# Kernel optimization log

Hardware: AMD Instinct MI355X
Metric: run time of the kernel (lower is better)

## Reference

```python
import jax, jax.numpy as jnp
import numpy as np

B, S, D, H = 4, 2048, 1024, 16
HS = D // H  # head_size = 64


def setup_inputs() -> dict:
    key = jax.random.key(0)
    ks = jax.random.split(key, 6)
    scale = 0.02
    return {
        "token_embeddings": jax.random.normal(ks[0], (B, S, D), dtype=jnp.float32),
        # per-head projection weights, stacked: [H, D, HS] (x @ W per head)
        "Wq": jax.random.normal(ks[1], (H, D, HS), dtype=jnp.float32) * scale,
        "Wk": jax.random.normal(ks[2], (H, D, HS), dtype=jnp.float32) * scale,
        "Wv": jax.random.normal(ks[3], (H, D, HS), dtype=jnp.float32) * scale,
        # output projection (Linear with bias): y = x @ Wo + bo
        "Wo": jax.random.normal(ks[4], (D, D), dtype=jnp.float32) * scale,
        "bo": jax.random.normal(ks[5], (D,), dtype=jnp.float32) * scale,
    }


def reference(token_embeddings, Wq, Wk, Wv, Wo, bo):
    # Per-head projections, batched over heads: [B,H,S,HS]
    q = jnp.einsum("bsd,hde->bhse", token_embeddings, Wq)
    k = jnp.einsum("bsd,hde->bhse", token_embeddings, Wk)
    v = jnp.einsum("bsd,hde->bhse", token_embeddings, Wv)
    scale = HS ** -0.5
    scores = jnp.einsum("bhqe,bhke->bhqk", q, k) * scale  # [B,H,S,S]
    causal = jnp.tril(jnp.ones((S, S), dtype=bool))
    scores = jnp.where(causal, scores, -jnp.inf)
    weights = jax.nn.softmax(scores, axis=-1)
    # dropout in eval mode -> identity
    out = jnp.einsum("bhqk,bhke->bhqe", weights, v)  # [B,H,S,HS]
    # concat heads -> [B,S,D] (head order matches torch.cat over heads)
    out = out.transpose(0, 2, 1, 3).reshape(B, S, D)
    return out @ Wo + bo
```

## Files before the change

kernel.cpp:

```cpp
#include <hip/hip_runtime.h>


typedef __bf16 bf16;
typedef bf16 bf16x8 __attribute__((ext_vector_type(8)));
typedef bf16 bf16x4 __attribute__((ext_vector_type(4)));
typedef float f32x4 __attribute__((ext_vector_type(4)));

__device__ __forceinline__ void gload16(const void* gsrc, void* ldst) {
  __builtin_amdgcn_global_load_lds(
      (const __attribute__((address_space(1))) unsigned int*)gsrc,
      (__attribute__((address_space(3))) unsigned int*)ldst, 16, 0, 0);
}

__device__ __forceinline__ f32x4 mfma16(bf16x8 a, bf16x8 b, f32x4 c) {
  return __builtin_amdgcn_mfma_f32_16x16x32_bf16(a, b, c, 0, 0, 0);
}

__global__ __launch_bounds__(256) void pack_x_kernel(const float* __restrict__ x,
                                                     bf16* __restrict__ xb) {
  int i = (blockIdx.x * 256 + threadIdx.x) * 4;
  float4 v = *(const float4*)(x + i);
  bf16x4 o;
  o[0] = (bf16)v.x; o[1] = (bf16)v.y; o[2] = (bf16)v.z; o[3] = (bf16)v.w;
  *(bf16x4*)(xb + i) = o;
}

__global__ __launch_bounds__(256) void pack_wqkv_kernel(const float* __restrict__ Wq,
                                                        const float* __restrict__ Wk,
                                                        const float* __restrict__ Wv,
                                                        bf16* __restrict__ WT) {
  int idx = blockIdx.x * 256 + threadIdx.x;
  int n = idx >> 10, k = idx & 1023;
  int sel = n >> 10, nn = n & 1023;
  const float* W = (sel == 0) ? Wq : (sel == 1 ? Wk : Wv);
  int h = nn >> 6, e = nn & 63;
  WT[(size_t)n * 1024 + k] = (bf16)W[h * 65536 + k * 64 + e];
}

__global__ __launch_bounds__(256) void pack_wo_kernel(const float* __restrict__ Wo,
                                                      bf16* __restrict__ WoT) {
  int idx = blockIdx.x * 256 + threadIdx.x;
  int n = idx >> 10, k = idx & 1023;
  WoT[idx] = (bf16)Wo[k * 1024 + n];
}

template <bool F32OUT>
__global__ __launch_bounds__(256, 2) void gemm4_kernel(const bf16* __restrict__ A,
                                                       const bf16* __restrict__ BT,
                                                       bf16* __restrict__ Cb,
                                                       float* __restrict__ Cf,
                                                       const float* __restrict__ bias,
                                                       int N, int K) {
  __shared__ bf16 As[2][128 * 64];
  __shared__ bf16 Bs[2][128 * 64];
  const int tid = threadIdx.x, lane = tid & 63, wave = tid >> 6;
  const int g = lane >> 4, c = lane & 15;
  const int wr = wave >> 1, wc = wave & 1;
  const int bid = blockIdx.x;
  const int xcd = bid & 7, local = bid >> 3;
  const int m0 = (xcd * 8 + (local & 7)) * 128;
  const int n0 = (local >> 3) * 128;

  const int schunk = (lane & 7) ^ (lane >> 3);

#define STAGE4(T, S)                                                      \
  do {                                                                    \
    _Pragma("unroll") for (int j = 0; j < 4; ++j) {                       \
      const int r = wave * 32 + j * 8 + (lane >> 3);                      \
      const int ldso = wave * 4096 + j * 1024 + lane * 16;                \
      gload16(A + (size_t)(m0 + r) * K + (T)*64 + schunk * 8,             \
              (char*)&As[S][0] + ldso);                                   \
      gload16(BT + (size_t)(n0 + r) * K + (T)*64 + schunk * 8,            \
              (char*)&Bs[S][0] + ldso);                                   \
    }                                                                     \
  } while (0)

  f32x4 acc[4][4] = {};
  const int nt = K >> 6;
  STAGE4(0, 0);
  asm volatile("s_waitcnt vmcnt(0)" ::: "memory");
  __builtin_amdgcn_sched_barrier(0);
  __builtin_amdgcn_s_barrier();
  __builtin_amdgcn_sched_barrier(0);

#pragma unroll 1
  for (int t = 0; t < nt; ++t) {
    const int s = t & 1;
    if (t + 1 < nt) STAGE4(t + 1, s ^ 1);
    bf16x8 af[4][2], bfr[4][2];
#pragma unroll
    for (int m = 0; m < 4; ++m) {
      const int row = wr * 64 + m * 16 + c;
#pragma unroll
      for (int kk = 0; kk < 2; ++kk)
        af[m][kk] = *(const bf16x8*)((const char*)&As[s][0] + row * 128 +
                                     (((kk * 4 + g) ^ (row & 7)) << 4));
    }
#pragma unroll
    for (int n = 0; n < 4; ++n) {
      const int row = wc * 64 + n * 16 + c;
#pragma unroll
      for (int kk = 0; kk < 2; ++kk)
        bfr[n][kk] = *(const bf16x8*)((const char*)&Bs[s][0] + row * 128 +
                                      (((kk * 4 + g) ^ (row & 7)) << 4));
    }
    asm volatile("s_waitcnt lgkmcnt(0)" ::: "memory");
    __builtin_amdgcn_sched_barrier(0);
    __builtin_amdgcn_s_setprio(1);
#pragma unroll
    for (int kk = 0; kk < 2; ++kk)
#pragma unroll
      for (int m = 0; m < 4; ++m)
#pragma unroll
        for (int n = 0; n < 4; ++n)
          acc[m][n] = mfma16(af[m][kk], bfr[n][kk], acc[m][n]);
    __builtin_amdgcn_s_setprio(0);
    __builtin_amdgcn_sched_barrier(0);
    if (t + 1 < nt) {
      asm volatile("s_waitcnt vmcnt(0)" ::: "memory");
      __builtin_amdgcn_sched_barrier(0);
      __builtin_amdgcn_s_barrier();
      __builtin_amdgcn_sched_barrier(0);
    }
  }
#undef STAGE4
#pragma unroll
  for (int m = 0; m < 4; ++m)
#pragma unroll
    for (int n = 0; n < 4; ++n)
#pragma unroll
      for (int i = 0; i < 4; ++i) {
        int row = m0 + wr * 64 + m * 16 + g * 4 + i;
        int col = n0 + wc * 64 + n * 16 + c;
        if (F32OUT)
          Cf[(size_t)row * N + col] = acc[m][n][i] + bias[col];
        else
          Cb[(size_t)row * N + col] = (bf16)acc[m][n][i];
      }
}

__global__ __launch_bounds__(256) void transpose_v_kernel(const bf16* __restrict__ qkv,
                                                          bf16* __restrict__ vt) {
  __shared__ bf16 tl[64][72];
  const int tid = threadIdx.x;
  const int st = blockIdx.x, bh = blockIdx.y;
  const int b = bh >> 4, h = bh & 15;
#pragma unroll
  for (int it = 0; it < 2; ++it) {
    int idx = it * 256 + tid;
    int sl = idx >> 3, ch = idx & 7;
    bf16x8 v = *(const bf16x8*)(qkv + (size_t)(b * 2048 + st * 64 + sl) * 3072 + 2048 + h * 64 + ch * 8);
    *(bf16x8*)&tl[sl][ch * 8] = v;
  }
  __syncthreads();
#pragma unroll
  for (int it = 0; it < 2; ++it) {
    int idx = it * 256 + tid;
    int d = idx >> 3, s8 = idx & 7;
    bf16x8 o;
#pragma unroll
    for (int j = 0; j < 8; ++j) o[j] = tl[s8 * 8 + j][d];
    *(bf16x8*)(vt + ((size_t)bh * 64 + d) * 2048 + st * 64 + s8 * 8) = o;
  }
}

__global__ __launch_bounds__(512, 4) void attn_kernel(const bf16* __restrict__ qkv,
                                                      const bf16* __restrict__ vt,
                                                      bf16* __restrict__ attn_out) {
  __shared__ bf16 Ks[2][128 * 64];
  __shared__ bf16 Vs[2][64 * 128];
  const int tid = threadIdx.x, lane = tid & 63, wave = tid >> 6;
  const int g = lane >> 4, c = lane & 15;
  const int bid = blockIdx.x;
  const int xcd = bid & 7;
  const int x = (bid >> 3) & 7;
  const int bh = (bid >> 6) * 8 + xcd;
  const int b = bh >> 4, h = bh & 15;
  const float SCL = 0.125f * 1.4426950408889634f;

  bf16x8 ones;
#pragma unroll
  for (int j = 0; j < 8; ++j) ones[j] = (bf16)1.0f;

#define STAGE(KT, BUF)                                                                    \
  do {                                                                                    \
    _Pragma("unroll") for (int t2 = 0; t2 < 2; ++t2) {                                    \
      int o = t2 * 8192 + wave * 1024 + lane * 16;                          \
      int rK = o >> 7, chK = (((o & 127) >> 4) ^ (rK & 7));                               \
      gload16((const char*)qkv +                                                          \
                  ((size_t)(b * 2048 + (KT)*128 + rK) * 3072 + 1024 + h * 64) * 2 +       \
                  (chK << 4),                                                             \
              (char*)Ks[BUF] + o);                                                        \
      int rV = o >> 8, chV = (((o & 255) >> 4) ^ (rV & 7));                               \
      gload16((const char*)vt + (((size_t)bh * 64 + rV) * 2048 + (KT)*128) * 2 +          \
                  (chV << 4),                                                             \
              (char*)Vs[BUF] + o);                                                        \
    }                                                                                     \
  } while (0)

#pragma unroll 1
  for (int ph = 0; ph < 2; ++ph) {
    const int qt = ph ? (15 - x) : x;
    const int qlow = qt * 128 + wave * 16;

    bf16x8 qf[2];
#pragma unroll
    for (int kk = 0; kk < 2; ++kk) {
      size_t row = (size_t)(b * 2048 + qlow + c);
      qf[kk] = *(const bf16x8*)(qkv + row * 3072 + h * 64 + kk * 32 + g * 8);
    }

    f32x4 oacc[4] = {};
    f32x4 lacc = {};
    float mrun = -3.0e38f;

    const int nkt = qt + 1;
    STAGE(0, 0);
    for (int kt = 0; kt < nkt; ++kt) {
      const int cur = kt & 1;
      if (kt + 1 < nkt) {
        STAGE(kt + 1, cur ^ 1);
        asm volatile("s_waitcnt vmcnt(4)" ::: "memory");
      } else {
        asm volatile("s_waitcnt vmcnt(0)" ::: "memory");
      }
      __builtin_amdgcn_sched_barrier(0);
      __builtin_amdgcn_s_barrier();
      __builtin_amdgcn_sched_barrier(0);
      f32x4 sc[8] = {};
      __builtin_amdgcn_s_setprio(1);
#pragma unroll
      for (int n = 0; n < 8; ++n) {
        int key = n * 16 + c;
#pragma unroll
        for (int kk = 0; kk < 2; ++kk) {
          bf16x8 kf = *(const bf16x8*)((const char*)Ks[cur] + key * 128 +
                                       (((kk * 4 + g) ^ (key & 7)) << 4));
          sc[n] = mfma16(kf, qf[kk], sc[n]);
        }
      }
      __builtin_amdgcn_s_setprio(0);
      const int q = qlow + c;
      if (kt == qt) {
#pragma unroll
        for (int n = 0; n < 8; ++n)
#pragma unroll
          for (int i = 0; i < 4; ++i)
            sc[n][i] = ((kt * 128 + n * 16 + 4 * g + i) <= q) ? sc[n][i] : -3.0e38f;
      }
      float vmax = -3.0e38f;
#pragma unroll
      for (int n = 0; n < 8; ++n)
#pragma unroll
        for (int i = 0; i < 4; ++i) vmax = fmaxf(vmax, sc[n][i]);
      vmax = fmaxf(vmax, __shfl_xor(vmax, 16));
      vmax = fmaxf(vmax, __shfl_xor(vmax, 32));
      const float mnew = fmaxf(mrun, vmax * SCL);
      const float fs = __builtin_amdgcn_exp2f(mrun - mnew);
      mrun = mnew;
#pragma unroll
      for (int n = 0; n < 8; ++n)
#pragma unroll
        for (int i = 0; i < 4; ++i)
          sc[n][i] = __builtin_amdgcn_exp2f(fmaf(sc[n][i], SCL, -mnew));
#pragma unroll
      for (int i = 0; i < 4; ++i) {
        float fsb = __shfl(fs, ((lane >> 4) << 2) + i);
        lacc[i] *= fsb;
#pragma unroll
        for (int dn = 0; dn < 4; ++dn) oacc[dn][i] *= fsb;
      }
      bf16x8 pa[4];
#pragma unroll
      for (int kss = 0; kss < 4; ++kss) {
        bf16x8 t;
#pragma unroll
        for (int j = 0; j < 4; ++j) t[j] = (bf16)sc[2 * kss][j];
#pragma unroll
        for (int j = 0; j < 4; ++j) t[4 + j] = (bf16)sc[2 * kss + 1][j];
        pa[kss] = t;
      }
      __builtin_amdgcn_s_setprio(1);
#pragma unroll
      for (int kss = 0; kss < 4; ++kss) {
        lacc = mfma16(pa[kss], ones, lacc);
#pragma unroll
        for (int dn = 0; dn < 4; ++dn) {
          const int d = dn * 16 + c;
          const char* vrow = (const char*)Vs[cur] + d * 256;
          const int off = 8 * (g & 1);
          bf16x4 lo = *(const bf16x4*)(vrow + (((4 * kss + (g >> 1)) ^ (d & 7)) << 4) + off);
          bf16x4 hi = *(const bf16x4*)(vrow + (((4 * kss + 2 + (g >> 1)) ^ (d & 7)) << 4) + off);
          bf16x8 vb;
#pragma unroll
          for (int j = 0; j < 4; ++j) { vb[j] = lo[j]; vb[4 + j] = hi[j]; }
          oacc[dn] = mfma16(pa[kss], vb, oacc[dn]);
        }
      }
      __builtin_amdgcn_s_setprio(0);
      __builtin_amdgcn_sched_barrier(0);
      __builtin_amdgcn_s_barrier();
      __builtin_amdgcn_sched_barrier(0);
    }
#pragma unroll
    for (int i = 0; i < 4; ++i) {
      float inv = __builtin_amdgcn_rcpf(lacc[i]);
      size_t row = (size_t)(b * 2048 + qlow + 4 * g + i);
#pragma unroll
      for (int dn = 0; dn < 4; ++dn)
        attn_out[row * 1024 + h * 64 + dn * 16 + c] = (bf16)(oacc[dn][i] * inv);
    }
  }
#undef STAGE
}

extern "C" void kernel_launch(void* const* d_in, const int* in_sizes, int n_in,
                              void* d_out, int out_size, void* d_ws, size_t ws_size,
                              hipStream_t stream) {
  const float* x  = (const float*)d_in[0];
  const float* Wq = (const float*)d_in[1];
  const float* Wk = (const float*)d_in[2];
  const float* Wv = (const float*)d_in[3];
  const float* Wo = (const float*)d_in[4];
  const float* bo = (const float*)d_in[5];
  float* out = (float*)d_out;
  char* ws = (char*)d_ws;

  bf16* Xb    = (bf16*)(ws);
  bf16* WqkvT = (bf16*)(ws + 16777216);
  bf16* WoT   = (bf16*)(ws + 23068672);
  bf16* QKV   = (bf16*)(ws + 25165824);
  bf16* VT    = (bf16*)(ws + 75497472);
  bf16* AttnO = (bf16*)(ws + 92274688);

  pack_x_kernel<<<8192, 256, 0, stream>>>(x, Xb);
  pack_wqkv_kernel<<<12288, 256, 0, stream>>>(Wq, Wk, Wv, WqkvT);
  pack_wo_kernel<<<4096, 256, 0, stream>>>(Wo, WoT);
  gemm4_kernel<false><<<1536, 256, 0, stream>>>(Xb, WqkvT, QKV, nullptr, nullptr,
                                                3072, 1024);
  transpose_v_kernel<<<dim3(32, 64), 256, 0, stream>>>(QKV, VT);
  attn_kernel<<<512, 512, 0, stream>>>(QKV, VT, AttnO);
  gemm4_kernel<true><<<512, 256, 0, stream>>>(AttnO, WoT, nullptr, out, bo,
                                              1024, 1024);
}
```

Baseline: 181.7 us.

## Pre-permute V transpose for single 16B LDS reads and add lazy softmax rescale

The V transpose kernel now writes keys in a permuted order that matches the MFMA operand layout. The attention inner loop can then fetch each V fragment with one 16-byte LDS read instead of two 8-byte reads plus a register shuffle. The running-max rescale of the accumulators is skipped unless some lane's new max exceeds the old one by more than 8 (in log2 units). This saves the shuffles and multiplies on most iterations, at the cost of a larger range of un-normalized exponentials in fp32/bf16. The row-max reduction is also rewritten as a tree to shorten the dependency chain.

```diff
diff --git a/kernel.cpp b/kernel.cpp
--- a/kernel.cpp
+++ b/kernel.cpp
@@ -156,11 +156,15 @@
 #pragma unroll
   for (int it = 0; it < 2; ++it) {
     int idx = it * 256 + tid;
-    int d = idx >> 3, s8 = idx & 7;
+    int d = idx >> 3, ch = idx & 7;
+    const int blk = ch >> 2, g = ch & 3;
     bf16x8 o;
 #pragma unroll
-    for (int j = 0; j < 8; ++j) o[j] = tl[s8 * 8 + j][d];
-    *(bf16x8*)(vt + ((size_t)bh * 64 + d) * 2048 + st * 64 + s8 * 8) = o;
+    for (int j = 0; j < 8; ++j) {
+      int loc = (j < 4) ? (4 * g + j) : (16 + 4 * g + (j - 4));
+      o[j] = tl[blk * 32 + loc][d];
+    }
+    *(bf16x8*)(vt + ((size_t)bh * 64 + d) * 2048 + st * 64 + ch * 8) = o;
   }
 }
 
@@ -248,28 +252,36 @@
           for (int i = 0; i < 4; ++i)
             sc[n][i] = ((kt * 128 + n * 16 + 4 * g + i) <= q) ? sc[n][i] : -3.0e38f;
       }
-      float vmax = -3.0e38f;
-#pragma unroll
-      for (int n = 0; n < 8; ++n)
-#pragma unroll
-        for (int i = 0; i < 4; ++i) vmax = fmaxf(vmax, sc[n][i]);
+      float vmax;
+      {
+        float a[8];
+#pragma unroll
+        for (int n = 0; n < 8; ++n)
+          a[n] = fmaxf(fmaxf(sc[n][0], sc[n][1]), fmaxf(sc[n][2], sc[n][3]));
+        float b0 = fmaxf(a[0], a[1]), b1 = fmaxf(a[2], a[3]);
+        float b2 = fmaxf(a[4], a[5]), b3 = fmaxf(a[6], a[7]);
+        vmax = fmaxf(fmaxf(b0, b1), fmaxf(b2, b3));
+      }
       vmax = fmaxf(vmax, __shfl_xor(vmax, 16));
       vmax = fmaxf(vmax, __shfl_xor(vmax, 32));
-      const float mnew = fmaxf(mrun, vmax * SCL);
-      const float fs = __builtin_amdgcn_exp2f(mrun - mnew);
-      mrun = mnew;
+      const float mx = vmax * SCL;
+      if (!__all(mx <= mrun + 8.0f)) {
+        const float mnew = fmaxf(mrun, mx);
+        const float fs = __builtin_amdgcn_exp2f(mrun - mnew);
+        mrun = mnew;
+#pragma unroll
+        for (int i = 0; i < 4; ++i) {
+          float fsb = __shfl(fs, ((lane >> 4) << 2) + i);
+          lacc[i] *= fsb;
+#pragma unroll
+          for (int dn = 0; dn < 4; ++dn) oacc[dn][i] *= fsb;
+        }
+      }
 #pragma unroll
       for (int n = 0; n < 8; ++n)
 #pragma unroll
         for (int i = 0; i < 4; ++i)
-          sc[n][i] = __builtin_amdgcn_exp2f(fmaf(sc[n][i], SCL, -mnew));
-#pragma unroll
-      for (int i = 0; i < 4; ++i) {
-        float fsb = __shfl(fs, ((lane >> 4) << 2) + i);
-        lacc[i] *= fsb;
-#pragma unroll
-        for (int dn = 0; dn < 4; ++dn) oacc[dn][i] *= fsb;
-      }
+          sc[n][i] = __builtin_amdgcn_exp2f(fmaf(sc[n][i], SCL, -mrun));
       bf16x8 pa[4];
 #pragma unroll
       for (int kss = 0; kss < 4; ++kss) {
@@ -287,13 +299,8 @@
 #pragma unroll
         for (int dn = 0; dn < 4; ++dn) {
           const int d = dn * 16 + c;
-          const char* vrow = (const char*)Vs[cur] + d * 256;
-          const int off = 8 * (g & 1);
-          bf16x4 lo = *(const bf16x4*)(vrow + (((4 * kss + (g >> 1)) ^ (d & 7)) << 4) + off);
-          bf16x4 hi = *(const bf16x4*)(vrow + (((4 * kss + 2 + (g >> 1)) ^ (d & 7)) << 4) + off);
-          bf16x8 vb;
-#pragma unroll
-          for (int j = 0; j < 4; ++j) { vb[j] = lo[j]; vb[4 + j] = hi[j]; }
+          bf16x8 vb = *(const bf16x8*)((const char*)Vs[cur] + d * 256 +
+                                       (((kss * 4 + g) ^ (d & 7)) << 4));
           oacc[dn] = mfma16(pa[kss], vb, oacc[dn]);
         }
       }
```

After: 172.5 us. 1.05x faster.
